# Optimization experiments

Measured on AMD Instinct MI355X. Metric: run time of the kernel, lower is better.

The kernel has to match this reference:

```python
import jax, jax.numpy as jnp
import numpy as np

D = 512
H = 8
DH = D // H
EPS = 1e-6


def _ln(x, g, b):
    m = x.mean(-1, keepdims=True)
    v = ((x - m) ** 2).mean(-1, keepdims=True)
    return g * (x - m) / jnp.sqrt(v + EPS) + b


def _mha(q_in, kv_in, W, B):
    # W: [4, D, D] = (Wq, Wk, Wv, Wo); B: [4, D]
    q = q_in @ W[0] + B[0]
    k = kv_in @ W[1] + B[1]
    v = kv_in @ W[2] + B[2]

    def split(t):
        b, l, _ = t.shape
        return t.reshape(b, l, H, DH).transpose(0, 2, 1, 3)  # [b,h,l,dh]

    q, k, v = split(q), split(k), split(v)
    s = jnp.einsum('bhqd,bhkd->bhqk', q, k) / np.sqrt(DH).astype(np.float32)
    a = jax.nn.softmax(s, axis=-1)
    o = jnp.einsum('bhqk,bhkd->bhqd', a, v)
    b_, _, l, _ = o.shape
    o = o.transpose(0, 2, 1, 3).reshape(b_, l, D)
    return o @ W[3] + B[3]


def _cross_layer(x, y, attn_w, attn_b, w1, b1, w2, b2, lns):
    # pre-norm residual sublayers (annotated-transformer style), dropout in eval mode
    x = x + _mha(_ln(x, lns[0, 0], lns[0, 1]), y, attn_w, attn_b)
    h = _ln(x, lns[1, 0], lns[1, 1])
    x = x + (jax.nn.relu(h @ w1 + b1) @ w2 + b2)
    return x


def _af(q, k, v, Wq, bq, Wo, bo):
    # AF with proj=True: single-head attention scaled by sqrt(embed_dim)
    q = q @ Wq + bq
    s = jnp.einsum('bqd,bkd->bqk', q, k) / np.sqrt(D).astype(np.float32)
    o = jax.nn.softmax(s, axis=-1) @ v
    return o @ Wo + bo


def _forward(x, text, vis,
             ft_attn_w, ft_attn_b, ft_w1, ft_b1, ft_w2, ft_b2, ft_ln,
             fv_attn_w, fv_attn_b, fv_w1, fv_b1, fv_w2, fv_b2, fv_ln,
             ldm_ln, af_w, af_b):
    # mode='y', proj=True path
    med = _cross_layer(vis, text, ft_attn_w, ft_attn_b, ft_w1, ft_b1, ft_w2, ft_b2, ft_ln)
    med = _cross_layer(med, vis, fv_attn_w, fv_attn_b, fv_w1, fv_b1, fv_w2, fv_b2, fv_ln) + med
    med = _ln(med, ldm_ln[0], ldm_ln[1])
    # FDIntervention: af_1(mediator, feature, feature) then af_2(feature, mediator, v)
    v = _af(med, x, x, af_w[0, 0], af_b[0, 0], af_w[0, 1], af_b[0, 1])
    out = _af(x, med, v, af_w[1, 0], af_b[1, 0], af_w[1, 1], af_b[1, 1])
    return out + x


def setup_inputs() -> dict:
    key = jax.random.key(0)
    ks = jax.random.split(key, 16)
    B, LX, LT, LV = 32, 256, 256, 196
    sc = 0.02

    def ln_pair():
        # [2(sublayers), 2(gamma,beta), D]
        return jnp.stack([jnp.stack([jnp.ones((D,)), jnp.zeros((D,))])] * 2)

    return {
        'x': jax.random.normal(ks[0], (B, LX, D), jnp.float32),
        'text': jax.random.normal(ks[1], (B, LT, D), jnp.float32),
        'vis': jax.random.normal(ks[2], (B, LV, D), jnp.float32),
        'ft_attn_w': jax.random.normal(ks[3], (4, D, D), jnp.float32) * sc,
        'ft_attn_b': jnp.zeros((4, D), jnp.float32),
        'ft_w1': jax.random.normal(ks[4], (D, 4 * D), jnp.float32) * sc,
        'ft_b1': jnp.zeros((4 * D,), jnp.float32),
        'ft_w2': jax.random.normal(ks[5], (4 * D, D), jnp.float32) * sc,
        'ft_b2': jnp.zeros((D,), jnp.float32),
        'ft_ln': ln_pair(),
        'fv_attn_w': jax.random.normal(ks[6], (4, D, D), jnp.float32) * sc,
        'fv_attn_b': jnp.zeros((4, D), jnp.float32),
        'fv_w1': jax.random.normal(ks[7], (D, 4 * D), jnp.float32) * sc,
        'fv_b1': jnp.zeros((4 * D,), jnp.float32),
        'fv_w2': jax.random.normal(ks[8], (4 * D, D), jnp.float32) * sc,
        'fv_b2': jnp.zeros((D,), jnp.float32),
        'fv_ln': ln_pair(),
        'ldm_ln': jnp.stack([jnp.ones((D,)), jnp.zeros((D,))]),
        'af_w': jax.random.normal(ks[9], (2, 2, D, D), jnp.float32) * sc,
        'af_b': jnp.zeros((2, 2, D), jnp.float32),
    }


def reference(x, text, vis,
              ft_attn_w, ft_attn_b, ft_w1, ft_b1, ft_w2, ft_b2, ft_ln,
              fv_attn_w, fv_attn_b, fv_w1, fv_b1, fv_w2, fv_b2, fv_ln,
              ldm_ln, af_w, af_b):
    return _forward(x, text, vis,
                    ft_attn_w, ft_attn_b, ft_w1, ft_b1, ft_w2, ft_b2, ft_ln,
                    fv_attn_w, fv_attn_b, fv_w1, fv_b1, fv_w2, fv_b2, fv_ln,
                    ldm_ln, af_w, af_b)
```

## Files before the change

### kernel.cpp

```cpp
#include <hip/hip_runtime.h>
#include <hip/hip_bf16.h>

typedef __attribute__((ext_vector_type(4))) float f32x4;
typedef __attribute__((ext_vector_type(8))) short s16x8;
typedef __attribute__((ext_vector_type(4))) short s16x4;

__device__ __forceinline__ short f2bf(float f) {
  union { float f; unsigned u; } c; c.f = f;
  unsigned r = c.u + 0x7fffu + ((c.u >> 16) & 1u);
  return (short)(r >> 16);
}
__device__ __forceinline__ float bf2f(short h) {
  union { unsigned u; float f; } c; c.u = ((unsigned)(unsigned short)h) << 16;
  return c.f;
}
__device__ __forceinline__ s16x8 cvt8(const f32x4& lo, const f32x4& hi) {
  s16x8 v;
  v[0] = f2bf(lo[0]); v[1] = f2bf(lo[1]); v[2] = f2bf(lo[2]); v[3] = f2bf(lo[3]);
  v[4] = f2bf(hi[0]); v[5] = f2bf(hi[1]); v[6] = f2bf(hi[2]); v[7] = f2bf(hi[3]);
  return v;
}

__device__ __forceinline__ void gl_lds16(const short* g, char* l) {
  __builtin_amdgcn_global_load_lds(
      (const __attribute__((address_space(1))) unsigned int*)g,
      (__attribute__((address_space(3))) unsigned int*)l, 16, 0, 0);
}

template<int CF32, int BM, int BN, int WRN, int WCN, int RING,
         int SM, int RELU, int NRES, int BIASM, int SWZ>
__global__ __launch_bounds__(WRN * WCN * 64, 2)
void gemm_k(const short* __restrict__ Ap, int hbA, long sAo, long sAi, int lda,
            const short* __restrict__ Bp, int hbB, long sBo, long sBi, int ldb,
            void* __restrict__ Cp, int hbC, long sCo, long sCi, int ldc,
            const float* __restrict__ bias,
            const float* __restrict__ res1,
            const float* __restrict__ res2,
            int M, int N, int K, float alpha, int nvalid)
{
  constexpr int WAVES = WRN * WCN;
  constexpr int T = WAVES * 64;
  constexpr int MI = BM / (WRN * 16), NI = BN / (WCN * 16);
  constexpr int ACH = BM * 8 / T, BCH = BN * 8 / T;
  constexpr int L   = ACH + BCH;
  constexpr int ABYTES = BM * 128;
  constexpr int TBYTES = (BM + BN) * 128;
  constexpr int LSTR = BN + (CF32 ? 4 : 8);
  constexpr int EPIB = BM * LSTR * (CF32 ? 4 : 2);
  constexpr int SMEMB = (RING * TBYTES > EPIB) ? RING * TBYTES : EPIB;
  __shared__ __align__(16) char smem[SMEMB];

  const int tid  = threadIdx.x;
  const int lane = tid & 63;
  const int wid  = tid >> 6;
  const int wr   = wid / WCN, wc = wid % WCN;

  int bx = blockIdx.x, by = blockIdx.y, bz = blockIdx.z;
  if constexpr (SWZ == 1) {
    const int gx = gridDim.x, gy = gridDim.y;
    const int nwg = gx * gy;
    const int o = by * gx + bx;
    const int q = nwg >> 3, r = nwg & 7;
    const int xcd = o & 7, slot = o >> 3;
    const int w = (xcd < r ? xcd * (q + 1) : r * (q + 1) + (xcd - r) * q) + slot;
    bx = w / gy; by = w - bx * gy;
  } else if constexpr (SWZ == 2) {
    const int gx = gridDim.x, gy = gridDim.y, gz = gridDim.z;
    const int nwg = gx * gy * gz;
    const int o = (bz * gy + by) * gx + bx;
    const int q = nwg >> 3, r = nwg & 7;
    const int xcd = o & 7, slot = o >> 3;
    int w = (xcd < r ? xcd * (q + 1) : r * (q + 1) + (xcd - r) * q) + slot;
    bx = w % gx; w /= gx; by = w % gy; bz = w / gy;
  }
  const int m0 = bx * BM, n0 = by * BN;
  const int z  = bz;

  const int zA = z / hbA, zAi = z - zA * hbA;
  const int zB = z / hbB, zBi = z - zB * hbB;
  const int zC = z / hbC, zCi = z - zC * hbC;
  const short* Ab = Ap + (long)zA * sAo + (long)zAi * sAi;
  const short* Bb = Bp + (long)zB * sBo + (long)zBi * sBi;
  char*        Cb = (char*)Cp + ((long)zC * sCo + (long)zCi * sCi) * (CF32 ? 4 : 2);

  int aL[ACH]; long aG[ACH];
#pragma unroll
  for (int j = 0; j < ACH; ++j) {
    int chunk = (j * WAVES + wid) * 64 + lane;
    int row = chunk >> 3;
    int c   = (chunk & 7) ^ (row & 7);
    int gr = m0 + row; if (gr > M - 1) gr = M - 1;
    aL[j] = chunk * 16;
    aG[j] = (long)gr * lda + c * 8;
  }
  int bL[BCH]; long bG[BCH];
#pragma unroll
  for (int j = 0; j < BCH; ++j) {
    int chunk = (j * WAVES + wid) * 64 + lane;
    int row = chunk >> 3;
    int c   = (chunk & 7) ^ (row & 7);
    int gc = n0 + row; if (gc > N - 1) gc = N - 1;
    bL[j] = chunk * 16;
    bG[j] = (long)gc * ldb + c * 8;
  }

  auto stage = [&](int buf, int kt) {
    const short* Akt = Ab + (long)kt * 64;
    char* base = smem + buf * TBYTES;
#pragma unroll
    for (int j = 0; j < ACH; ++j) gl_lds16(Akt + aG[j], base + aL[j]);
    const short* Bkt = Bb + (long)kt * 64;
#pragma unroll
    for (int j = 0; j < BCH; ++j) gl_lds16(Bkt + bG[j], base + ABYTES + bL[j]);
  };

  int ard[2][MI], brd[2][NI];
#pragma unroll
  for (int kk = 0; kk < 2; ++kk) {
    int kgr = kk * 4 + (lane >> 4);
#pragma unroll
    for (int mi = 0; mi < MI; ++mi) {
      int m = wr * (BM / WRN) + mi * 16 + (lane & 15);
      ard[kk][mi] = m * 128 + ((kgr ^ (m & 7)) << 4);
    }
#pragma unroll
    for (int ni = 0; ni < NI; ++ni) {
      int n = wc * (BN / WCN) + ni * 16 + (lane & 15);
      brd[kk][ni] = ABYTES + n * 128 + ((kgr ^ (n & 7)) << 4);
    }
  }

  const int NT = K >> 6;
#pragma unroll
  for (int p = 0; p < RING; ++p) if (p < NT) stage(p, p);

  f32x4 acc[MI][NI];
#pragma unroll
  for (int mi = 0; mi < MI; ++mi)
#pragma unroll
    for (int ni = 0; ni < NI; ++ni) acc[mi][ni] = (f32x4){0.f, 0.f, 0.f, 0.f};

  int bufi = 0;
  for (int t = 0; t < NT; ++t) {
    const int rem = NT - t;
    if constexpr (RING == 3) {
      if (rem >= 3)      asm volatile("s_waitcnt vmcnt(%0)" :: "n"(2 * L) : "memory");
      else if (rem == 2) asm volatile("s_waitcnt vmcnt(%0)" :: "n"(L) : "memory");
      else               asm volatile("s_waitcnt vmcnt(0)" ::: "memory");
    } else if constexpr (RING == 2) {
      if (rem >= 2)      asm volatile("s_waitcnt vmcnt(%0)" :: "n"(L) : "memory");
      else               asm volatile("s_waitcnt vmcnt(0)" ::: "memory");
    } else {
      asm volatile("s_waitcnt vmcnt(0)" ::: "memory");
    }
    asm volatile("s_barrier" ::: "memory");

    const char* base = smem + bufi * TBYTES;
#pragma unroll
    for (int kk = 0; kk < 2; ++kk) {
      s16x8 af[MI];
#pragma unroll
      for (int mi = 0; mi < MI; ++mi) af[mi] = *(const s16x8*)(base + ard[kk][mi]);
#pragma unroll
      for (int ni = 0; ni < NI; ++ni) {
        s16x8 bf = *(const s16x8*)(base + brd[kk][ni]);
#pragma unroll
        for (int mi = 0; mi < MI; ++mi)
          acc[mi][ni] = __builtin_amdgcn_mfma_f32_16x16x32_bf16(af[mi], bf, acc[mi][ni], 0, 0, 0);
      }
    }

    if (t + RING < NT) {
      asm volatile("s_waitcnt lgkmcnt(0)" ::: "memory");
      asm volatile("s_barrier" ::: "memory");
      stage(bufi, t + RING);
    }
    bufi = (bufi + 1 == RING) ? 0 : bufi + 1;
  }

  if constexpr (SM) {
#pragma unroll
    for (int mi = 0; mi < MI; ++mi) {
#pragma unroll
      for (int j = 0; j < 4; ++j) {
        float mx = -3.0e38f;
#pragma unroll
        for (int ni = 0; ni < NI; ++ni) {
          int col = n0 + wc * (BN / WCN) + ni * 16 + (lane & 15);
          float s = acc[mi][ni][j] * alpha;
          acc[mi][ni][j] = (col < nvalid) ? s : -3.0e38f;
          mx = fmaxf(mx, acc[mi][ni][j]);
        }
#pragma unroll
        for (int o = 1; o < 16; o <<= 1) mx = fmaxf(mx, __shfl_xor(mx, o));
        float sum = 0.f;
#pragma unroll
        for (int ni = 0; ni < NI; ++ni) {
          int col = n0 + wc * (BN / WCN) + ni * 16 + (lane & 15);
          float e = (col < nvalid) ? __expf(acc[mi][ni][j] - mx) : 0.f;
          acc[mi][ni][j] = e;
          sum += e;
        }
#pragma unroll
        for (int o = 1; o < 16; o <<= 1) sum += __shfl_xor(sum, o);
        float inv = 1.f / sum;
#pragma unroll
        for (int ni = 0; ni < NI; ++ni) acc[mi][ni][j] *= inv;
      }
    }
  }
  const float aep = SM ? 1.f : alpha;

  asm volatile("s_waitcnt lgkmcnt(0)" ::: "memory");
  __syncthreads();

  {
    float* lf = (float*)smem;
    short* lh = (short*)smem;
#pragma unroll
    for (int mi = 0; mi < MI; ++mi)
#pragma unroll
      for (int ni = 0; ni < NI; ++ni) {
        int c_loc = wc * (BN / WCN) + ni * 16 + (lane & 15);
        float bv = (bias && !BIASM) ? bias[n0 + c_loc] : 0.f;
        int rb = wr * (BM / WRN) + mi * 16 + ((lane >> 4) << 2);
#pragma unroll
        for (int j = 0; j < 4; ++j) {
          float v = acc[mi][ni][j] * aep + bv;
          if constexpr (CF32) lf[(rb + j) * LSTR + c_loc] = v;
          else                lh[(rb + j) * LSTR + c_loc] = f2bf(v);
        }
      }
  }
  __syncthreads();

  constexpr int CPR = BN / 8;
  constexpr int RP  = T / CPR;
  const int rr0 = tid / CPR;
  const int cc  = (tid % CPR) * 8;
  for (int r = rr0; r < BM; r += RP) {
    const int gr = m0 + r;
    if (gr >= M) break;
    f32x4 a, b;
    if constexpr (CF32) {
      a = *(const f32x4*)((const float*)smem + (long)r * LSTR + cc);
      b = *(const f32x4*)((const float*)smem + (long)r * LSTR + cc + 4);
    } else {
      s16x8 h = *(const s16x8*)((const short*)smem + (long)r * LSTR + cc);
#pragma unroll
      for (int j = 0; j < 4; ++j) { a[j] = bf2f(h[j]); b[j] = bf2f(h[j + 4]); }
    }
    if constexpr (BIASM) {
      float bm = bias[gr];
#pragma unroll
      for (int j = 0; j < 4; ++j) { a[j] += bm; b[j] += bm; }
    }
    const long gb = (long)gr * ldc + n0 + cc;
    if constexpr (NRES >= 1) {
      f32x4 r1 = *(const f32x4*)(res1 + gb), r2 = *(const f32x4*)(res1 + gb + 4);
#pragma unroll
      for (int j = 0; j < 4; ++j) { a[j] += r1[j]; b[j] += r2[j]; }
    }
    if constexpr (NRES >= 2) {
      f32x4 r1 = *(const f32x4*)(res2 + gb), r2 = *(const f32x4*)(res2 + gb + 4);
#pragma unroll
      for (int j = 0; j < 4; ++j) { a[j] += r1[j]; b[j] += r2[j]; }
    }
    if constexpr (RELU) {
#pragma unroll
      for (int j = 0; j < 4; ++j) { a[j] = fmaxf(a[j], 0.f); b[j] = fmaxf(b[j], 0.f); }
    }
    if constexpr (CF32) {
      *(f32x4*)((float*)Cb + gb) = a;
      *(f32x4*)((float*)Cb + gb + 4) = b;
    } else {
      *(s16x8*)((short*)Cb + gb) = cvt8(a, b);
    }
  }
}

__global__ __launch_bounds__(256, 2)
void mha_k(const short* __restrict__ Qp, long qStride,
           const short* __restrict__ Kp, long kStride, int ldk, int Lkv,
           const short* __restrict__ VTp, long vtStride,
           short* __restrict__ Op, int Lq, float alpha, int nvalid)
{
  __shared__ __align__(16) char smem[73728];
  char* Qs  = smem;
  char* Ks  = smem + 8192;
  char* VTs = smem + 40960;

  const int tid = threadIdx.x, lane = tid & 63, wid = tid >> 6;

  int bxr = blockIdx.x, bzr = blockIdx.z;
  {
    const int gx = gridDim.x, gz = gridDim.z;
    const int nwg = gx * gz;
    const int o = bzr * gx + bxr;
    const int q = nwg >> 3, r = nwg & 7;
    const int xcd = o & 7, slot = o >> 3;
    int w = (xcd < r ? xcd * (q + 1) : r * (q + 1) + (xcd - r) * q) + slot;
    bxr = w % gx; bzr = w / gx;
  }
  const int z = bzr, b = z >> 3, h = z & 7;
  const int m0 = bxr * 64;

  const short* Qb  = Qp + (long)b * qStride + h * 64;
  const short* Kb  = Kp + (long)b * kStride + h * 64;
  const short* VTb = VTp + (long)z * vtStride;
  short*       Ob  = Op + (long)b * qStride + h * 64;

#pragma unroll
  for (int j = 0; j < 2; ++j) {
    int chunk = (j * 4 + wid) * 64 + lane;
    int row = chunk >> 3, c = (chunk & 7) ^ (row & 7);
    int gr = m0 + row; if (gr > Lq - 1) gr = Lq - 1;
    gl_lds16(Qb + (long)gr * 512 + c * 8, Qs + chunk * 16);
  }
#pragma unroll
  for (int j = 0; j < 8; ++j) {
    int chunk = (j * 4 + wid) * 64 + lane;
    int row = chunk >> 3, c = (chunk & 7) ^ (row & 7);
    int gr = row; if (gr > Lkv - 1) gr = Lkv - 1;
    gl_lds16(Kb + (long)gr * ldk + c * 8, Ks + chunk * 16);
  }
#pragma unroll
  for (int j = 0; j < 8; ++j) {
    int chunk = (j * 4 + wid) * 64 + lane;
    int row = chunk >> 5, cw = (chunk & 31) ^ (row & 15);
    gl_lds16(VTb + (long)row * 256 + cw * 8, VTs + chunk * 16);
  }
  __syncthreads();

  f32x4 acc[16];
#pragma unroll
  for (int ni = 0; ni < 16; ++ni) acc[ni] = (f32x4){0.f, 0.f, 0.f, 0.f};
#pragma unroll
  for (int kk = 0; kk < 2; ++kk) {
    int kgr = kk * 4 + (lane >> 4);
    int m = wid * 16 + (lane & 15);
    s16x8 af = *(const s16x8*)(Qs + m * 128 + ((kgr ^ (m & 7)) << 4));
#pragma unroll
    for (int ni = 0; ni < 16; ++ni) {
      int n = ni * 16 + (lane & 15);
      s16x8 bf = *(const s16x8*)(Ks + n * 128 + ((kgr ^ (n & 7)) << 4));
      acc[ni] = __builtin_amdgcn_mfma_f32_16x16x32_bf16(af, bf, acc[ni], 0, 0, 0);
    }
  }

#pragma unroll
  for (int j = 0; j < 4; ++j) {
    float mx = -3.0e38f;
#pragma unroll
    for (int ni = 0; ni < 16; ++ni) {
      int col = ni * 16 + (lane & 15);
      float s = acc[ni][j] * alpha;
      acc[ni][j] = (col < nvalid) ? s : -3.0e38f;
      mx = fmaxf(mx, acc[ni][j]);
    }
#pragma unroll
    for (int o = 1; o < 16; o <<= 1) mx = fmaxf(mx, __shfl_xor(mx, o));
    float sum = 0.f;
#pragma unroll
    for (int ni = 0; ni < 16; ++ni) {
      int col = ni * 16 + (lane & 15);
      float e = (col < nvalid) ? __expf(acc[ni][j] - mx) : 0.f;
      acc[ni][j] = e;
      sum += e;
    }
#pragma unroll
    for (int o = 1; o < 16; o <<= 1) sum += __shfl_xor(sum, o);
    float inv = 1.f / sum;
#pragma unroll
    for (int ni = 0; ni < 16; ++ni) acc[ni][j] *= inv;
  }

  __syncthreads();

  {
    char* Ps = Ks + wid * 8192;
    const int r0 = (lane >> 4) * 4;
#pragma unroll
    for (int ni = 0; ni < 16; ++ni) {
      int col = ni * 16 + (lane & 15);
      int chunk = col >> 3, cin = (col & 7) * 2;
#pragma unroll
      for (int j = 0; j < 4; ++j) {
        int row = r0 + j;
        *(short*)(Ps + row * 512 + ((chunk ^ (row & 15)) << 4) + cin) = f2bf(acc[ni][j]);
      }
    }
  }
  asm volatile("s_waitcnt lgkmcnt(0)" ::: "memory");

  f32x4 acco[4];
#pragma unroll
  for (int ni = 0; ni < 4; ++ni) acco[ni] = (f32x4){0.f, 0.f, 0.f, 0.f};
  {
    const char* Ps = Ks + wid * 8192;
#pragma unroll
    for (int kk = 0; kk < 8; ++kk) {
      int g = lane >> 4;
      int mrow = lane & 15;
      int achunk = (kk * 4 + g) ^ (mrow & 15);
      s16x8 af = *(const s16x8*)(Ps + mrow * 512 + (achunk << 4));
#pragma unroll
      for (int ni = 0; ni < 4; ++ni) {
        int n = ni * 16 + (lane & 15);
        int bchunk = (kk * 4 + g) ^ (n & 15);
        s16x8 bf = *(const s16x8*)(VTs + n * 512 + (bchunk << 4));
        acco[ni] = __builtin_amdgcn_mfma_f32_16x16x32_bf16(af, bf, acco[ni], 0, 0, 0);
      }
    }
  }

  __syncthreads();

  {
    short* lh = (short*)smem;
#pragma unroll
    for (int ni = 0; ni < 4; ++ni) {
      int d = ni * 16 + (lane & 15);
      int rb = wid * 16 + ((lane >> 4) << 2);
#pragma unroll
      for (int j = 0; j < 4; ++j) lh[(rb + j) * 72 + d] = f2bf(acco[ni][j]);
    }
  }
  __syncthreads();
  {
    const int r0 = tid >> 3, cc = (tid & 7) * 8;
#pragma unroll
    for (int p = 0; p < 2; ++p) {
      int r = r0 + p * 32;
      int gr = m0 + r;
      if (gr < Lq) {
        s16x8 h8 = *(const s16x8*)((const short*)smem + r * 72 + cc);
        *(s16x8*)(Ob + (long)gr * 512 + cc) = h8;
      }
    }
  }
}

__global__ __launch_bounds__(256)
void transpose_k(const short* __restrict__ inp, short* __restrict__ outp,
                 int R_in, int rs_in, int Rpad, int tiles_r,
                 int hb, long sO, long sI, long out_bs)
{
  __shared__ float tile[64][65];
  const int z = blockIdx.y;
  const int zo = z / hb, zi = z - zo * hb;
  const short* in = inp + (long)zo * sO + (long)zi * sI;
  short* out = outp + (long)z * out_bs;
  const int zt = blockIdx.x;
  const int tr = zt % tiles_r, tc = zt / tiles_r;
  const int r0 = tr * 64, c0 = tc * 64;
  const int c = threadIdx.x & 63, l0 = threadIdx.x >> 6;

#pragma unroll 4
  for (int i = 0; i < 16; ++i) {
    int l = l0 + i * 4;
    int gr = r0 + l;
    float v = 0.f;
    if (gr < R_in) v = bf2f(in[(long)gr * rs_in + c0 + c]);
    tile[l][c] = v;
  }
  __syncthreads();
#pragma unroll 4
  for (int i = 0; i < 16; ++i) {
    int cr = l0 + i * 4;
    out[(long)(c0 + cr) * Rpad + r0 + c] = f2bf(tile[c][cr]);
  }
}

__global__ __launch_bounds__(256)
void transposeWall_k(const float* ftw, const float* fvw, const float* afw,
                     const float* ftw1, const float* fvw1,
                     const float* ftw2, const float* fvw2,
                     short* wTbase, short* dW1, short* dW2)
{
  __shared__ float tile[64][65];
  const int z = blockIdx.y, zt = blockIdx.x;
  const float* in; short* out;
  int R_in, rs_in, Rpad, tiles_r;
  if (z < 12) {
    if (zt >= 64) return;
    const int grp = z >> 2, idx = z & 3;
    in = (grp == 0 ? ftw : grp == 1 ? fvw : afw) + (long)idx * 262144;
    out = wTbase + (long)grp * 3145728 + (long)idx * 262144;
    R_in = 512; rs_in = 512; Rpad = 512; tiles_r = 8;
  } else if (z < 14) {
    const int idx = z - 12;
    in = (idx == 0 ? ftw1 : fvw1);
    out = (idx == 0 ? dW1 : dW1 + 3145728);
    R_in = 512; rs_in = 2048; Rpad = 512; tiles_r = 8;
  } else {
    const int idx = z - 14;
    in = (idx == 0 ? ftw2 : fvw2);
    out = (idx == 0 ? dW2 : dW2 + 3145728);
    R_in = 2048; rs_in = 512; Rpad = 2048; tiles_r = 32;
  }
  const int tr = zt % tiles_r, tc = zt / tiles_r;
  const int r0 = tr * 64, c0 = tc * 64;
  const int c = threadIdx.x & 63, l0 = threadIdx.x >> 6;

#pragma unroll 4
  for (int i = 0; i < 16; ++i) {
    int l = l0 + i * 4;
    int gr = r0 + l;
    float v = 0.f;
    if (gr < R_in) v = in[(long)gr * rs_in + c0 + c];
    tile[l][c] = v;
  }
  __syncthreads();
#pragma unroll 4
  for (int i = 0; i < 16; ++i) {
    int cr = l0 + i * 4;
    out[(long)(c0 + cr) * Rpad + r0 + c] = f2bf(tile[c][cr]);
  }
}

__global__ __launch_bounds__(256)
void cvt2_k(const float* __restrict__ a, short* __restrict__ oa, long na,
            const float* __restrict__ b, short* __restrict__ ob, long nb)
{
  long i = ((long)blockIdx.x * 256 + threadIdx.x) * 8;
  const float* src; short* dst;
  if (i < na) { src = a + i; dst = oa + i; }
  else if (i < na + nb) { src = b + (i - na); dst = ob + (i - na); }
  else return;
  f32x4 lo = *(const f32x4*)src, hi = *(const f32x4*)(src + 4);
  *(s16x8*)dst = cvt8(lo, hi);
}

template<int RAW>
__global__ __launch_bounds__(256)
void ln_k(const float* __restrict__ in, const float* __restrict__ g,
          const float* __restrict__ b, short* __restrict__ outp,
          short* __restrict__ rawp, int rows)
{
  int row = blockIdx.x * 4 + (threadIdx.x >> 6);
  if (row >= rows) return;
  int lane = threadIdx.x & 63;
  const float* p = in + (long)row * 512 + lane * 8;
  f32x4 v0 = *(const f32x4*)p, v1 = *(const f32x4*)(p + 4);
  if constexpr (RAW) {
    short* rp = rawp + (long)row * 512 + lane * 8;
    *(s16x8*)rp = cvt8(v0, v1);
  }
  float s = 0.f, sq = 0.f;
#pragma unroll
  for (int j = 0; j < 4; ++j) { s += v0[j] + v1[j]; sq += v0[j]*v0[j] + v1[j]*v1[j]; }
#pragma unroll
  for (int o = 1; o < 64; o <<= 1) { s += __shfl_xor(s, o); sq += __shfl_xor(sq, o); }
  float mean = s * (1.f / 512.f);
  float var  = sq * (1.f / 512.f) - mean * mean;
  float rs   = rsqrtf(var + 1e-6f);
  const f32x4 g0 = *(const f32x4*)(g + lane * 8), g1 = *(const f32x4*)(g + lane * 8 + 4);
  const f32x4 b0 = *(const f32x4*)(b + lane * 8), b1 = *(const f32x4*)(b + lane * 8 + 4);
  f32x4 o0, o1;
#pragma unroll
  for (int j = 0; j < 4; ++j) {
    o0[j] = g0[j] * (v0[j] - mean) * rs + b0[j];
    o1[j] = g1[j] * (v1[j] - mean) * rs + b1[j];
  }
  short* op = outp + (long)row * 512 + lane * 8;
  *(s16x8*)op = cvt8(o0, o1);
}

static inline int ceildiv(int a, int b) { return (a + b - 1) / b; }

template<int CF32, int BM, int BN, int WRN, int WCN, int RING,
         int SM, int RELU, int NRES, int BIASM, int SWZ>
static void launch_gemm(hipStream_t st, int gm, int gn, int gz,
                        const short* A, int hbA, long sAo, long sAi, int lda,
                        const short* B, int hbB, long sBo, long sBi, int ldb,
                        void* C, int hbC, long sCo, long sCi, int ldc,
                        const float* bias, const float* r1, const float* r2,
                        int M, int N, int K, float alpha, int nvalid)
{
  gemm_k<CF32, BM, BN, WRN, WCN, RING, SM, RELU, NRES, BIASM, SWZ>
      <<<dim3(gm, gn, gz), dim3(WRN * WCN * 64), 0, st>>>(
          A, hbA, sAo, sAi, lda, B, hbB, sBo, sBi, ldb,
          C, hbC, sCo, sCi, ldc, bias, r1, r2, M, N, K, alpha, nvalid);
}

extern "C" void kernel_launch(void* const* d_in, const int* in_sizes, int n_in,
                              void* d_out, int out_size, void* d_ws, size_t ws_size,
                              hipStream_t stream)
{
  (void)in_sizes; (void)n_in; (void)out_size; (void)ws_size;

  const float* x     = (const float*)d_in[0];
  const float* text  = (const float*)d_in[1];
  const float* vis   = (const float*)d_in[2];
  const float* ftw   = (const float*)d_in[3];
  const float* ftb   = (const float*)d_in[4];
  const float* ftw1  = (const float*)d_in[5];
  const float* ftb1  = (const float*)d_in[6];
  const float* ftw2  = (const float*)d_in[7];
  const float* ftb2  = (const float*)d_in[8];
  const float* ftln  = (const float*)d_in[9];
  const float* fvw   = (const float*)d_in[10];
  const float* fvb   = (const float*)d_in[11];
  const float* fvw1  = (const float*)d_in[12];
  const float* fvb1  = (const float*)d_in[13];
  const float* fvw2  = (const float*)d_in[14];
  const float* fvb2  = (const float*)d_in[15];
  const float* fvln  = (const float*)d_in[16];
  const float* ldmln = (const float*)d_in[17];
  const float* afw   = (const float*)d_in[18];
  const float* afb   = (const float*)d_in[19];
  float* out = (float*)d_out;

  char* ws = (char*)d_ws;
  short* wT     = (short*)ws;
  short* xbf    = (short*)(ws + 14680064);
  short* bufLN  = (short*)(ws + 23068672);
  short* bufQ   = (short*)(ws + 29491200);
  short* bufKV  = (short*)(ws + 37879808);
  short* bufT   = (short*)(ws + 54657024);
  short* bufS   = (short*)(ws + 63045632);
  short* bufO   = (short*)(ws + 88735744);
  float* bufX1  = (float*)(ws + 97124352);
  float* bufA2  = (float*)(ws + 109969408);
  short* bufMED = (short*)(ws + 122814464);
  short* textbf = bufO;
  short* visbf  = (short*)bufA2;

  short* ftWq  = wT + 0;
  short* ftWk  = wT + 262144;
  short* ftWo  = wT + 786432;
  short* ftW1t = wT + 1048576;
  short* ftW2t = wT + 2097152;
  short* fvWq  = wT + 3145728;
  short* fvWk  = wT + 3407872;
  short* fvWo  = wT + 3932160;
  short* fvW1t = wT + 4194304;
  short* fvW2t = wT + 5242880;
  short* afW00 = wT + 6291456;
  short* afW01 = wT + 6553600;
  short* afW10 = wT + 6815744;
  short* afW11 = wT + 7077888;

  const float AFS = 0.04419417382415922f;
  dim3 blk(256);

  transposeWall_k<<<dim3(256, 16), blk, 0, stream>>>(
      ftw, fvw, afw, ftw1, fvw1, ftw2, fvw2, wT, ftW1t, ftW2t);
  cvt2_k<<<4096, blk, 0, stream>>>(x, xbf, 4194304L, text, textbf, 4194304L);

  ln_k<1><<<1568, blk, 0, stream>>>(vis, ftln + 0, ftln + 512, bufLN, visbf, 6272);
  launch_gemm<0,128,64,2,2,3,0,0,0,0,1>(stream, 49,8,1, bufLN,1,0,0,512, ftWq,1,0,0,512,
      bufQ,1,0,0,512, ftb + 0, nullptr, nullptr, 6272,512,512, 1.f, 0);
  launch_gemm<0,128,128,2,2,2,0,0,0,0,1>(stream, 64,8,1, textbf,1,0,0,512, ftWk,1,0,0,512,
      bufKV,1,0,0,1024, ftb + 512, nullptr, nullptr, 8192,1024,512, 1.f, 0);
  transpose_k<<<dim3(4,256), blk, 0, stream>>>(bufKV + 512, bufT, 256, 1024, 256, 4, 8, 262144L, 64L, 16384L);
  mha_k<<<dim3(4,1,256), blk, 0, stream>>>(bufQ, 100352L, bufKV, 262144L, 1024, 256,
      bufT, 16384L, bufO, 196, 0.125f, 256);
  launch_gemm<1,128,64,2,2,3,0,0,1,0,1>(stream, 49,8,1, bufO,1,0,0,512, ftWo,1,0,0,512,
      bufX1,1,0,0,512, ftb + 1536, vis, nullptr, 6272,512,512, 1.f, 0);
  ln_k<0><<<1568, blk, 0, stream>>>(bufX1, ftln + 1024, ftln + 1536, bufLN, nullptr, 6272);
  launch_gemm<0,128,128,2,2,2,0,1,0,0,1>(stream, 49,16,1, bufLN,1,0,0,512, ftW1t,1,0,0,512,
      bufS,1,0,0,2048, ftb1, nullptr, nullptr, 6272,2048,512, 1.f, 0);
  launch_gemm<1,128,64,2,2,3,0,0,1,0,1>(stream, 49,8,1, bufS,1,0,0,2048, ftW2t,1,0,0,2048,
      bufX1,1,0,0,512, ftb2, bufX1, nullptr, 6272,512,2048, 1.f, 0);

  ln_k<0><<<1568, blk, 0, stream>>>(bufX1, fvln + 0, fvln + 512, bufLN, nullptr, 6272);
  launch_gemm<0,128,64,2,2,3,0,0,0,0,1>(stream, 49,8,1, bufLN,1,0,0,512, fvWq,1,0,0,512,
      bufQ,1,0,0,512, fvb + 0, nullptr, nullptr, 6272,512,512, 1.f, 0);
  launch_gemm<0,128,128,2,2,2,0,0,0,0,1>(stream, 49,8,1, visbf,1,0,0,512, fvWk,1,0,0,512,
      bufKV,1,0,0,1024, fvb + 512, nullptr, nullptr, 6272,1024,512, 1.f, 0);
  transpose_k<<<dim3(4,256), blk, 0, stream>>>(bufKV + 512, bufT, 196, 1024, 256, 4, 8, 200704L, 64L, 16384L);
  mha_k<<<dim3(4,1,256), blk, 0, stream>>>(bufQ, 100352L, bufKV, 200704L, 1024, 196,
      bufT, 16384L, bufO, 196, 0.125f, 196);
  launch_gemm<1,128,64,2,2,3,0,0,1,0,1>(stream, 49,8,1, bufO,1,0,0,512, fvWo,1,0,0,512,
      bufA2,1,0,0,512, fvb + 1536, bufX1, nullptr, 6272,512,512, 1.f, 0);
  ln_k<0><<<1568, blk, 0, stream>>>(bufA2, fvln + 1024, fvln + 1536, bufLN, nullptr, 6272);
  launch_gemm<0,128,128,2,2,2,0,1,0,0,1>(stream, 49,16,1, bufLN,1,0,0,512, fvW1t,1,0,0,512,
      bufS,1,0,0,2048, fvb1, nullptr, nullptr, 6272,2048,512, 1.f, 0);
  launch_gemm<1,128,64,2,2,3,0,0,2,0,1>(stream, 49,8,1, bufS,1,0,0,2048, fvW2t,1,0,0,2048,
      bufA2,1,0,0,512, fvb2, bufA2, bufX1, 6272,512,2048, 1.f, 0);
  ln_k<0><<<1568, blk, 0, stream>>>(bufA2, ldmln + 0, ldmln + 512, bufMED, nullptr, 6272);

  transpose_k<<<dim3(32,32), blk, 0, stream>>>(xbf, bufT, 256, 512, 256, 4, 1, 131072L, 0L, 131072L);
  launch_gemm<0,128,64,2,2,3,0,0,0,0,1>(stream, 49,8,1, bufMED,1,0,0,512, afW00,1,0,0,512,
      bufQ,1,0,0,512, afb + 0, nullptr, nullptr, 6272,512,512, 1.f, 0);
  launch_gemm<0,32,256,2,1,2,1,0,0,0,2>(stream, 7,1,32, bufQ,1,100352L,0L,512, xbf,1,131072L,0L,512,
      bufS,1,50176L,0L,256, nullptr, nullptr, nullptr, 196,256,512, AFS, 256);
  launch_gemm<0,64,128,2,2,3,0,0,0,0,2>(stream, 4,4,32, bufS,1,50176L,0L,256, bufT,1,131072L,0L,256,
      bufO,1,100352L,0L,512, nullptr, nullptr, nullptr, 196,512,256, 1.f, 0);
  launch_gemm<0,128,64,2,2,3,0,0,0,1,2>(stream, 4,4,32, afW01,1,0,0,512, bufO,1,100352L,0L,512,
      bufT,1,131072L,0L,256, afb + 512, nullptr, nullptr, 512,256,512, 1.f, 0);

  launch_gemm<0,128,64,2,2,3,0,0,0,0,1>(stream, 64,8,1, xbf,1,0,0,512, afW10,1,0,0,512,
      bufQ,1,0,0,512, afb + 1024, nullptr, nullptr, 8192,512,512, 1.f, 0);
  launch_gemm<0,32,256,2,1,2,1,0,0,0,2>(stream, 8,1,32, bufQ,1,131072L,0L,512, bufMED,1,100352L,0L,512,
      bufS,1,65536L,0L,256, nullptr, nullptr, nullptr, 256,256,512, AFS, 196);
  launch_gemm<0,64,128,2,2,3,0,0,0,0,2>(stream, 4,4,32, bufS,1,65536L,0L,256, bufT,1,131072L,0L,256,
      bufO,1,131072L,0L,512, nullptr, nullptr, nullptr, 256,512,256, 1.f, 0);
  launch_gemm<1,128,64,2,2,3,0,0,1,0,1>(stream, 64,8,1, bufO,1,0,0,512, afW11,1,0,0,512,
      out,1,0,0,512, afb + 1536, x, nullptr, 8192,512,512, 1.f, 0);
}
```

Before: 374.1 us.

## Compute V projection directly transposed and merge prep kernels into one launch

```diff
diff --git a/kernel.cpp b/kernel.cpp
--- a/kernel.cpp
+++ b/kernel.cpp
@@ -442,44 +442,25 @@
 }
 
 __global__ __launch_bounds__(256)
-void transpose_k(const short* __restrict__ inp, short* __restrict__ outp,
-                 int R_in, int rs_in, int Rpad, int tiles_r,
-                 int hb, long sO, long sI, long out_bs)
+void prep_k(const float* ftw, const float* fvw, const float* afw,
+            const float* ftw1, const float* fvw1,
+            const float* ftw2, const float* fvw2,
+            const float* x, const float* text,
+            short* wTbase, short* dW1, short* dW2,
+            short* xbf, short* textbf, short* xT)
 {
+  const int z = blockIdx.y, zt = blockIdx.x;
+
+  if (z >= 16 && z < 32) {
+    long off = (long)(z & 7) * 524288 + (long)zt * 2048 + threadIdx.x * 8;
+    const float* src = (z < 24 ? x : text) + off;
+    short* dst = (z < 24 ? xbf : textbf) + off;
+    f32x4 lo = *(const f32x4*)src, hi = *(const f32x4*)(src + 4);
+    *(s16x8*)dst = cvt8(lo, hi);
+    return;
+  }
+
   __shared__ float tile[64][65];
-  const int z = blockIdx.y;
-  const int zo = z / hb, zi = z - zo * hb;
-  const short* in = inp + (long)zo * sO + (long)zi * sI;
-  short* out = outp + (long)z * out_bs;
-  const int zt = blockIdx.x;
-  const int tr = zt % tiles_r, tc = zt / tiles_r;
-  const int r0 = tr * 64, c0 = tc * 64;
-  const int c = threadIdx.x & 63, l0 = threadIdx.x >> 6;
-
-#pragma unroll 4
-  for (int i = 0; i < 16; ++i) {
-    int l = l0 + i * 4;
-    int gr = r0 + l;
-    float v = 0.f;
-    if (gr < R_in) v = bf2f(in[(long)gr * rs_in + c0 + c]);
-    tile[l][c] = v;
-  }
-  __syncthreads();
-#pragma unroll 4
-  for (int i = 0; i < 16; ++i) {
-    int cr = l0 + i * 4;
-    out[(long)(c0 + cr) * Rpad + r0 + c] = f2bf(tile[c][cr]);
-  }
-}
-
-__global__ __launch_bounds__(256)
-void transposeWall_k(const float* ftw, const float* fvw, const float* afw,
-                     const float* ftw1, const float* fvw1,
-                     const float* ftw2, const float* fvw2,
-                     short* wTbase, short* dW1, short* dW2)
-{
-  __shared__ float tile[64][65];
-  const int z = blockIdx.y, zt = blockIdx.x;
   const float* in; short* out;
   int R_in, rs_in, Rpad, tiles_r;
   if (z < 12) {
@@ -493,11 +474,17 @@
     in = (idx == 0 ? ftw1 : fvw1);
     out = (idx == 0 ? dW1 : dW1 + 3145728);
     R_in = 512; rs_in = 2048; Rpad = 512; tiles_r = 8;
-  } else {
+  } else if (z < 16) {
     const int idx = z - 14;
     in = (idx == 0 ? ftw2 : fvw2);
     out = (idx == 0 ? dW2 : dW2 + 3145728);
     R_in = 2048; rs_in = 512; Rpad = 2048; tiles_r = 32;
+  } else {
+    if (zt >= 32) return;
+    const int b = z - 32;
+    in = x + (long)b * 131072;
+    out = xT + (long)b * 131072;
+    R_in = 256; rs_in = 512; Rpad = 256; tiles_r = 4;
   }
   const int tr = zt % tiles_r, tc = zt / tiles_r;
   const int r0 = tr * 64, c0 = tc * 64;
@@ -517,19 +504,6 @@
     int cr = l0 + i * 4;
     out[(long)(c0 + cr) * Rpad + r0 + c] = f2bf(tile[c][cr]);
   }
-}
-
-__global__ __launch_bounds__(256)
-void cvt2_k(const float* __restrict__ a, short* __restrict__ oa, long na,
-            const float* __restrict__ b, short* __restrict__ ob, long nb)
-{
-  long i = ((long)blockIdx.x * 256 + threadIdx.x) * 8;
-  const float* src; short* dst;
-  if (i < na) { src = a + i; dst = oa + i; }
-  else if (i < na + nb) { src = b + (i - na); dst = ob + (i - na); }
-  else return;
-  f32x4 lo = *(const f32x4*)src, hi = *(const f32x4*)(src + 4);
-  *(s16x8*)dst = cvt8(lo, hi);
 }
 
 template<int RAW>
@@ -624,16 +598,19 @@
   float* bufX1  = (float*)(ws + 97124352);
   float* bufA2  = (float*)(ws + 109969408);
   short* bufMED = (short*)(ws + 122814464);
+  short* bufT2  = (short*)(ws + 129236992);
   short* textbf = bufO;
   short* visbf  = (short*)bufA2;
 
   short* ftWq  = wT + 0;
   short* ftWk  = wT + 262144;
+  short* ftWv  = wT + 524288;
   short* ftWo  = wT + 786432;
   short* ftW1t = wT + 1048576;
   short* ftW2t = wT + 2097152;
   short* fvWq  = wT + 3145728;
   short* fvWk  = wT + 3407872;
+  short* fvWv  = wT + 3670016;
   short* fvWo  = wT + 3932160;
   short* fvW1t = wT + 4194304;
   short* fvW2t = wT + 5242880;
@@ -645,17 +622,18 @@
   const float AFS = 0.04419417382415922f;
   dim3 blk(256);
 
-  transposeWall_k<<<dim3(256, 16), blk, 0, stream>>>(
-      ftw, fvw, afw, ftw1, fvw1, ftw2, fvw2, wT, ftW1t, ftW2t);
-  cvt2_k<<<4096, blk, 0, stream>>>(x, xbf, 4194304L, text, textbf, 4194304L);
+  prep_k<<<dim3(256, 64), blk, 0, stream>>>(
+      ftw, fvw, afw, ftw1, fvw1, ftw2, fvw2, x, text,
+      wT, ftW1t, ftW2t, xbf, textbf, bufT2);
 
   ln_k<1><<<1568, blk, 0, stream>>>(vis, ftln + 0, ftln + 512, bufLN, visbf, 6272);
   launch_gemm<0,128,64,2,2,3,0,0,0,0,1>(stream, 49,8,1, bufLN,1,0,0,512, ftWq,1,0,0,512,
       bufQ,1,0,0,512, ftb + 0, nullptr, nullptr, 6272,512,512, 1.f, 0);
-  launch_gemm<0,128,128,2,2,2,0,0,0,0,1>(stream, 64,8,1, textbf,1,0,0,512, ftWk,1,0,0,512,
-      bufKV,1,0,0,1024, ftb + 512, nullptr, nullptr, 8192,1024,512, 1.f, 0);
-  transpose_k<<<dim3(4,256), blk, 0, stream>>>(bufKV + 512, bufT, 256, 1024, 256, 4, 8, 262144L, 64L, 16384L);
-  mha_k<<<dim3(4,1,256), blk, 0, stream>>>(bufQ, 100352L, bufKV, 262144L, 1024, 256,
+  launch_gemm<0,128,64,2,2,3,0,0,0,0,1>(stream, 64,8,1, textbf,1,0,0,512, ftWk,1,0,0,512,
+      bufKV,1,0,0,512, ftb + 512, nullptr, nullptr, 8192,512,512, 1.f, 0);
+  launch_gemm<0,128,64,2,2,3,0,0,0,1,2>(stream, 4,4,32, ftWv,1,0,0,512, textbf,1,131072L,0L,512,
+      bufT,1,131072L,0L,256, ftb + 1024, nullptr, nullptr, 512,256,512, 1.f, 0);
+  mha_k<<<dim3(4,1,256), blk, 0, stream>>>(bufQ, 100352L, bufKV, 131072L, 512, 256,
       bufT, 16384L, bufO, 196, 0.125f, 256);
   launch_gemm<1,128,64,2,2,3,0,0,1,0,1>(stream, 49,8,1, bufO,1,0,0,512, ftWo,1,0,0,512,
       bufX1,1,0,0,512, ftb + 1536, vis, nullptr, 6272,512,512, 1.f, 0);
@@ -668,10 +646,11 @@
   ln_k<0><<<1568, blk, 0, stream>>>(bufX1, fvln + 0, fvln + 512, bufLN, nullptr, 6272);
   launch_gemm<0,128,64,2,2,3,0,0,0,0,1>(stream, 49,8,1, bufLN,1,0,0,512, fvWq,1,0,0,512,
       bufQ,1,0,0,512, fvb + 0, nullptr, nullptr, 6272,512,512, 1.f, 0);
-  launch_gemm<0,128,128,2,2,2,0,0,0,0,1>(stream, 49,8,1, visbf,1,0,0,512, fvWk,1,0,0,512,
-      bufKV,1,0,0,1024, fvb + 512, nullptr, nullptr, 6272,1024,512, 1.f, 0);
-  transpose_k<<<dim3(4,256), blk, 0, stream>>>(bufKV + 512, bufT, 196, 1024, 256, 4, 8, 200704L, 64L, 16384L);
-  mha_k<<<dim3(4,1,256), blk, 0, stream>>>(bufQ, 100352L, bufKV, 200704L, 1024, 196,
+  launch_gemm<0,128,64,2,2,3,0,0,0,0,1>(stream, 49,8,1, visbf,1,0,0,512, fvWk,1,0,0,512,
+      bufKV,1,0,0,512, fvb + 512, nullptr, nullptr, 6272,512,512, 1.f, 0);
+  launch_gemm<0,128,64,2,2,3,0,0,0,1,2>(stream, 4,4,32, fvWv,1,0,0,512, visbf,1,100352L,0L,512,
+      bufT,1,131072L,0L,256, fvb + 1024, nullptr, nullptr, 512,196,512, 1.f, 0);
+  mha_k<<<dim3(4,1,256), blk, 0, stream>>>(bufQ, 100352L, bufKV, 100352L, 512, 196,
       bufT, 16384L, bufO, 196, 0.125f, 196);
   launch_gemm<1,128,64,2,2,3,0,0,1,0,1>(stream, 49,8,1, bufO,1,0,0,512, fvWo,1,0,0,512,
       bufA2,1,0,0,512, fvb + 1536, bufX1, nullptr, 6272,512,512, 1.f, 0);
@@ -682,12 +661,11 @@
       bufA2,1,0,0,512, fvb2, bufA2, bufX1, 6272,512,2048, 1.f, 0);
   ln_k<0><<<1568, blk, 0, stream>>>(bufA2, ldmln + 0, ldmln + 512, bufMED, nullptr, 6272);
 
-  transpose_k<<<dim3(32,32), blk, 0, stream>>>(xbf, bufT, 256, 512, 256, 4, 1, 131072L, 0L, 131072L);
   launch_gemm<0,128,64,2,2,3,0,0,0,0,1>(stream, 49,8,1, bufMED,1,0,0,512, afW00,1,0,0,512,
       bufQ,1,0,0,512, afb + 0, nullptr, nullptr, 6272,512,512, 1.f, 0);
   launch_gemm<0,32,256,2,1,2,1,0,0,0,2>(stream, 7,1,32, bufQ,1,100352L,0L,512, xbf,1,131072L,0L,512,
       bufS,1,50176L,0L,256, nullptr, nullptr, nullptr, 196,256,512, AFS, 256);
-  launch_gemm<0,64,128,2,2,3,0,0,0,0,2>(stream, 4,4,32, bufS,1,50176L,0L,256, bufT,1,131072L,0L,256,
+  launch_gemm<0,64,128,2,2,3,0,0,0,0,2>(stream, 4,4,32, bufS,1,50176L,0L,256, bufT2,1,131072L,0L,256,
       bufO,1,100352L,0L,512, nullptr, nullptr, nullptr, 196,512,256, 1.f, 0);
   launch_gemm<0,128,64,2,2,3,0,0,0,1,2>(stream, 4,4,32, afW01,1,0,0,512, bufO,1,100352L,0L,512,
       bufT,1,131072L,0L,256, afb + 512, nullptr, nullptr, 512,256,512, 1.f, 0);
```

New measurement: 358.4 us. -4.2%, faster.
